# Optimization experiments

Measured on AMD Instinct MI355X. Metric: run time of the kernel, lower is better.

## Reference

```python
import jax, jax.numpy as jnp
import numpy as np
from jax import lax

B, CIN, L = 2048, 1024, 30
E, C = 8, 2            # num_experts, num_classes
FC_IN = 256 * 9        # 2304
FIN_IN = C + 512 * L + 256 * (L // 2 + 1)  # 19458


def _maxpool1d(x):
    # MaxPool1d(kernel=2, stride=2, padding=1); pad with -inf like torch
    return lax.reduce_window(x, -jnp.inf, lax.max,
                             (1, 1, 2), (1, 1, 2),
                             [(0, 0), (0, 0), (1, 1)])


def _conv1d(x, w):
    # x: [B,Cin,L], w: [Cout,Cin,3], padding=1
    return lax.conv_general_dilated(x, w, (1,), [(1, 1)],
                                    dimension_numbers=('NCH', 'OIH', 'NCH'))


def setup_inputs() -> dict:
    key = jax.random.key(0)
    ks = jax.random.split(key, 16)
    s = 0.02
    inp = {
        'x': jax.random.normal(ks[0], (B, CIN, L), jnp.float32),
        'expert_idx': jax.random.randint(ks[1], (B,), 0, E),
        'conv1_w': jax.random.normal(ks[2], (512, 1024, 3), jnp.float32) * s,
        'conv1_b': jnp.zeros((512,), jnp.float32),
        'conv2_w': jax.random.normal(ks[3], (256, 512, 3), jnp.float32) * s,
        'conv2_b': jnp.zeros((256,), jnp.float32),
        'fc_w': jax.random.normal(ks[4], (1024, FC_IN), jnp.float32) * s,
        'fc_b': jnp.zeros((1024,), jnp.float32),
        'e_w1': jax.random.normal(ks[5], (E, 512, 1024), jnp.float32) * s,
        'e_b1': jnp.zeros((E, 512), jnp.float32),
        'e_w2': jax.random.normal(ks[6], (E, C, 512), jnp.float32) * s,
        'e_b2': jnp.zeros((E, C), jnp.float32),
        'agg_w': jax.random.normal(ks[7], (C, E * C), jnp.float32) * s,
        'agg_b': jnp.zeros((C,), jnp.float32),
        'fin_w': jax.random.normal(ks[8], (C, FIN_IN), jnp.float32) * s,
        'fin_b': jnp.zeros((C,), jnp.float32),
    }
    return inp


def reference(x, expert_idx, conv1_w, conv1_b, conv2_w, conv2_b, fc_w, fc_b,
              e_w1, e_b1, e_w2, e_b2, agg_w, agg_b, fin_w, fin_b):
    b = x.shape[0]
    # shared feature extractor
    x1 = jax.nn.relu(_conv1d(x, conv1_w) + conv1_b[None, :, None])     # [B,512,30]
    p1 = _maxpool1d(x1)                                                 # [B,512,16]
    x2 = jax.nn.relu(_conv1d(p1, conv2_w) + conv2_b[None, :, None])    # [B,256,16]
    p2 = _maxpool1d(x2)                                                 # [B,256,9]
    sf = jax.nn.relu(p2.reshape(b, -1) @ fc_w.T + fc_b)                 # [B,1024]

    # expert dispatch: run all experts densely, then select per-sample
    h = jax.nn.relu(jnp.einsum('bd,ehd->beh', sf, e_w1) + e_b1)        # [B,E,512]
    all_out = jnp.einsum('beh,ech->bec', h, e_w2) + e_b2               # [B,E,C]
    sel = all_out[jnp.arange(b), expert_idx]                           # [B,C]
    oh = jax.nn.one_hot(expert_idx, E, dtype=sel.dtype)                # [B,E]
    expert_outputs = (oh[:, :, None] * sel[:, None, :]).reshape(b, E * C)

    agg = expert_outputs @ agg_w.T + agg_b                             # [B,C]
    combined = jnp.concatenate(
        [agg, x1.reshape(b, -1), x2.reshape(b, -1)], axis=1)           # [B,19458]
    return combined @ fin_w.T + fin_b                                  # [B,C]
```

## Files before the change

kernel.cpp:

```cpp
#include <hip/hip_runtime.h>
#include <hip/hip_bf16.h>

typedef short short8 __attribute__((ext_vector_type(8)));
typedef short short4v __attribute__((ext_vector_type(4)));
typedef float f32x4 __attribute__((ext_vector_type(4)));

__device__ __forceinline__ float bf2f(short s) {
  return __builtin_bit_cast(float, (unsigned)((unsigned short)s) << 16);
}
__device__ __forceinline__ short f2bf(float f) {
  return __builtin_bit_cast(short, __float2bfloat16(f));
}
__device__ __forceinline__ void g2lds16(const void* g, void* l) {
  __builtin_amdgcn_global_load_lds((const __attribute__((address_space(1))) void*)g,
                                   (__attribute__((address_space(3))) void*)l, 16, 0, 0);
}


__global__ __launch_bounds__(256) void prep_x(const float* __restrict__ x, short* __restrict__ xt) {
  __shared__ float tile[64 * 30];
  const int b = blockIdx.x, ci0 = blockIdx.y * 64, t = threadIdx.x;
  const float* src = x + ((long)b * 1024 + ci0) * 30;
  for (int i = t; i < 480; i += 256)
    ((float4*)tile)[i] = ((const float4*)src)[i];
  __syncthreads();
  short* dst = xt + (long)b * 32 * 1024 + ci0;
  for (int i = t; i < 512; i += 256) {
    int lp = i >> 4, cq = i & 15;
    short4v v = {0, 0, 0, 0};
    if (lp >= 1 && lp <= 30) {
#pragma unroll
      for (int u = 0; u < 4; ++u) v[u] = f2bf(tile[(cq * 4 + u) * 30 + lp - 1]);
    }
    *(short4v*)&dst[(long)lp * 1024 + cq * 4] = v;
  }
}

__global__ __launch_bounds__(256) void prep_weights(
    const float* __restrict__ conv1_w, const float* __restrict__ conv2_w,
    const float* __restrict__ fc_w, const float* __restrict__ e_w1,
    const float* __restrict__ fin_w,
    short* __restrict__ w1t, short* __restrict__ w2t, short* __restrict__ fcwt,
    short* __restrict__ ew1t, float* __restrict__ finw1, float* __restrict__ finw2) {
  const int T0 = 1572864;
  const int T1 = T0 + 393216;
  const int T2 = T1 + 2359296;
  const int T3 = T2 + 4194304;
  const int T4 = T3 + 30720;
  const int T5 = T4 + 8192;
  for (long idx = (long)blockIdx.x * 256 + threadIdx.x; idx < T5;
       idx += (long)gridDim.x * 256) {
    if (idx < T0) {
      int i = (int)idx; int co = i / 3072, j = i % 3072, k = j >> 10, ci = j & 1023;
      w1t[i] = f2bf(conv1_w[(co * 1024 + ci) * 3 + k]);
    } else if (idx < T1) {
      int i = (int)(idx - T0); int co = i / 1536, j = i % 1536, k = j >> 9, ci = j & 511;
      w2t[i] = f2bf(conv2_w[(co * 512 + ci) * 3 + k]);
    } else if (idx < T2) {
      int i = (int)(idx - T1); int n = i / 2304, j = i % 2304, jj = j >> 8, co = j & 255;
      fcwt[i] = f2bf(fc_w[n * 2304 + co * 9 + jj]);
    } else if (idx < T3) {
      int i = (int)(idx - T2);
      ew1t[i] = f2bf(e_w1[i]);
    } else if (idx < T4) {
      int i = (int)(idx - T3); int c = i / 15360, r = i % 15360, l = r >> 9, co = r & 511;
      finw1[i] = fin_w[c * 19458 + 2 + co * 30 + l];
    } else {
      int i = (int)(idx - T4); int c = i / 4096, r = i % 4096, l = r >> 8, co = r & 255;
      finw2[i] = fin_w[c * 19458 + 2 + 15360 + co * 16 + l];
    }
  }
}

__global__ __launch_bounds__(512, 2) void gemm256_bt_relu(
    const short* __restrict__ A, const short* __restrict__ Bm, short* __restrict__ C,
    const float* __restrict__ bias, int N, int K, int L, int S1, int S2, int nNB) {
  __shared__ __align__(16) short lA0[256 * 64], lA1[256 * 64];
  __shared__ __align__(16) short lB0[256 * 64], lB1[256 * 64];
  const int t = threadIdx.x, wave = t >> 6, lane = t & 63;
  const int wr = wave >> 2, wc = wave & 3;
  const int nwg = gridDim.x, qn = nwg >> 3, bid = blockIdx.x;
  const int swz = (bid & 7) * qn + (bid >> 3);
  const int m0 = (swz / nNB) * 256, n0 = (swz % nNB) * 256;
  const int srow = t >> 3;
  const int scol = (((t & 7) ^ (srow & 7)) * 8);

  long aoff[4], boff[4];
#pragma unroll
  for (int q = 0; q < 4; ++q) {
    int m = m0 + q * 64 + srow;
    aoff[q] = (long)(m / L) * S1 + (long)(m % L) * S2 + scol;
    boff[q] = (long)(n0 + q * 64 + srow) * K + scol;
  }
  const int ldst = wave * 512 + lane * 8;

  f32x4 acc[8][4];
#pragma unroll
  for (int i = 0; i < 8; ++i)
#pragma unroll
    for (int j = 0; j < 4; ++j) acc[i][j] = f32x4{0.f, 0.f, 0.f, 0.f};

  const int l7 = lane & 7, g4 = lane >> 4, r16 = lane & 15;
  const int nK = K >> 6;

#define STAGE256(k0, dA, dB) do {                                     \
    const long kk0_ = (long)(k0);                                     \
    _Pragma("unroll")                                                 \
    for (int q = 0; q < 4; ++q) {                                     \
      g2lds16(A + aoff[q] + kk0_, &dA[q * 4096 + ldst]);              \
      g2lds16(Bm + boff[q] + kk0_, &dB[q * 4096 + ldst]);             \
    } } while (0)

#define PHASES256(sA, sB) do {                                                        \
    short8 af[4][2], bfr[4][2];                                                       \
                                 \
    _Pragma("unroll") for (int kk = 0; kk < 2; ++kk) {                                \
      const int jb = ((kk * 4 + g4) ^ l7) * 8;                                        \
      _Pragma("unroll") for (int i = 0; i < 4; ++i)                                   \
        af[i][kk] = *(const short8*)&sA[(wr * 128 + i * 16 + r16) * 64 + jb];         \
      _Pragma("unroll") for (int j = 0; j < 2; ++j)                                   \
        bfr[j][kk] = *(const short8*)&sB[(wc * 64 + j * 16 + r16) * 64 + jb];         \
    }                                                                                 \
    __builtin_amdgcn_s_setprio(1);                                                    \
    _Pragma("unroll") for (int i = 0; i < 4; ++i)                                     \
    _Pragma("unroll") for (int j = 0; j < 2; ++j)                                     \
    _Pragma("unroll") for (int kk = 0; kk < 2; ++kk)                                  \
      acc[i][j] = __builtin_amdgcn_mfma_f32_16x16x32_bf16(af[i][kk], bfr[j][kk], acc[i][j], 0, 0, 0); \
    __builtin_amdgcn_s_setprio(0);                                                    \
                                         \
    _Pragma("unroll") for (int kk = 0; kk < 2; ++kk) {                                \
      const int jb = ((kk * 4 + g4) ^ l7) * 8;                                        \
      _Pragma("unroll") for (int j = 0; j < 2; ++j)                                   \
        bfr[2 + j][kk] = *(const short8*)&sB[(wc * 64 + (2 + j) * 16 + r16) * 64 + jb]; \
    }                                                                                 \
    __builtin_amdgcn_s_setprio(1);                                                    \
    _Pragma("unroll") for (int i = 0; i < 4; ++i)                                     \
    _Pragma("unroll") for (int j = 0; j < 2; ++j)                                     \
    _Pragma("unroll") for (int kk = 0; kk < 2; ++kk)                                  \
      acc[i][2 + j] = __builtin_amdgcn_mfma_f32_16x16x32_bf16(af[i][kk], bfr[2 + j][kk], acc[i][2 + j], 0, 0, 0); \
    __builtin_amdgcn_s_setprio(0);                                                    \
                                         \
    _Pragma("unroll") for (int kk = 0; kk < 2; ++kk) {                                \
      const int jb = ((kk * 4 + g4) ^ l7) * 8;                                        \
      _Pragma("unroll") for (int i = 0; i < 4; ++i)                                   \
        af[i][kk] = *(const short8*)&sA[(wr * 128 + (4 + i) * 16 + r16) * 64 + jb];   \
    }                                                                                 \
    __builtin_amdgcn_s_setprio(1);                                                    \
    _Pragma("unroll") for (int i = 0; i < 4; ++i)                                     \
    _Pragma("unroll") for (int j = 0; j < 2; ++j)                                     \
    _Pragma("unroll") for (int kk = 0; kk < 2; ++kk)                                  \
      acc[4 + i][2 + j] = __builtin_amdgcn_mfma_f32_16x16x32_bf16(af[i][kk], bfr[2 + j][kk], acc[4 + i][2 + j], 0, 0, 0); \
    __builtin_amdgcn_s_setprio(0);                                                    \
                                \
    __builtin_amdgcn_s_setprio(1);                                                    \
    _Pragma("unroll") for (int i = 0; i < 4; ++i)                                     \
    _Pragma("unroll") for (int j = 0; j < 2; ++j)                                     \
    _Pragma("unroll") for (int kk = 0; kk < 2; ++kk)                                  \
      acc[4 + i][j] = __builtin_amdgcn_mfma_f32_16x16x32_bf16(af[i][kk], bfr[j][kk], acc[4 + i][j], 0, 0, 0); \
    __builtin_amdgcn_s_setprio(0);                                                    \
  } while (0)

  STAGE256(0, lA0, lB0);
  for (int ktp = 0; ktp < (nK >> 1); ++ktp) {
    const int t1 = 2 * ktp + 1;
    __syncthreads();
    STAGE256((long)t1 << 6, lA1, lB1);
    PHASES256(lA0, lB0);
    __syncthreads();
    if (t1 + 1 < nK) STAGE256((long)(t1 + 1) << 6, lA0, lB0);
    PHASES256(lA1, lB1);
  }

#pragma unroll
  for (int j = 0; j < 4; ++j) {
    int col = n0 + wc * 64 + j * 16 + r16;
    float bv = bias[col];
#pragma unroll
    for (int i = 0; i < 8; ++i) {
      int rbase = m0 + wr * 128 + i * 16 + (g4 << 2);
#pragma unroll
      for (int r = 0; r < 4; ++r) {
        float o = fmaxf(acc[i][j][r] + bv, 0.f);
        C[(long)(rbase + r) * N + col] = f2bf(o);
      }
    }
  }
#undef STAGE256
#undef PHASES256
}

__global__ __launch_bounds__(256, 2) void gemm128_bt_relu(
    const short* __restrict__ A, const short* __restrict__ Bm, short* __restrict__ C,
    const float* __restrict__ bias, int N, int K, int L, int S1, int S2, int nNB) {
  __shared__ __align__(16) short lA0[128 * 64], lA1[128 * 64];
  __shared__ __align__(16) short lB0[128 * 64], lB1[128 * 64];
  const int t = threadIdx.x, wave = t >> 6, lane = t & 63;
  const int wr = wave >> 1, wc = wave & 1;
  const int nwg = gridDim.x, qn = nwg >> 3, bid = blockIdx.x;
  const int swz = (bid & 7) * qn + (bid >> 3);
  const int m0 = (swz / nNB) * 128, n0 = (swz % nNB) * 128;
  const int arow = t >> 3;
  const int acolg = (((t & 7) ^ (arow & 7)) * 8);

  long aoff[4], boff[4];
#pragma unroll
  for (int qq = 0; qq < 4; ++qq) {
    int m = m0 + qq * 32 + arow;
    aoff[qq] = (long)(m / L) * S1 + (long)(m % L) * S2 + acolg;
    boff[qq] = (long)(n0 + qq * 32 + arow) * K + acolg;
  }
  const int ldst = wave * 512 + lane * 8;

  f32x4 acc[4][4];
#pragma unroll
  for (int i = 0; i < 4; ++i)
#pragma unroll
    for (int j = 0; j < 4; ++j) acc[i][j] = f32x4{0.f, 0.f, 0.f, 0.f};

  const int l7 = lane & 7, g4 = lane >> 4, r16 = lane & 15;
  const int nK = K >> 6;

#define STAGE128(k0, dA, dB) do {                                     \
    const long kk0_ = (long)(k0);                                     \
    _Pragma("unroll")                                                 \
    for (int qq = 0; qq < 4; ++qq) {                                  \
      g2lds16(A + aoff[qq] + kk0_, &dA[qq * 2048 + ldst]);            \
      g2lds16(Bm + boff[qq] + kk0_, &dB[qq * 2048 + ldst]);           \
    } } while (0)

#define PHASES128(sA, sB) do {                                                        \
    _Pragma("unroll")                                                                 \
    for (int kk = 0; kk < 2; ++kk) {                                                  \
      const int jblk = ((kk * 4 + g4) ^ l7) * 8;                                      \
      short8 af[4], bfv[4];                                                           \
      _Pragma("unroll") for (int i = 0; i < 4; ++i)                                   \
        af[i] = *(const short8*)&sA[(wr * 64 + i * 16 + r16) * 64 + jblk];            \
      _Pragma("unroll") for (int j = 0; j < 4; ++j)                                   \
        bfv[j] = *(const short8*)&sB[(wc * 64 + j * 16 + r16) * 64 + jblk];           \
      __builtin_amdgcn_s_setprio(1);                                                  \
      _Pragma("unroll") for (int i = 0; i < 4; ++i)                                   \
      _Pragma("unroll") for (int j = 0; j < 4; ++j)                                   \
        acc[i][j] = __builtin_amdgcn_mfma_f32_16x16x32_bf16(af[i], bfv[j], acc[i][j], 0, 0, 0); \
      __builtin_amdgcn_s_setprio(0);                                                  \
    } } while (0)

  STAGE128(0, lA0, lB0);
  for (int ktp = 0; ktp < (nK >> 1); ++ktp) {
    const int t1 = 2 * ktp + 1;
    __syncthreads();
    STAGE128((long)t1 << 6, lA1, lB1);
    PHASES128(lA0, lB0);
    __syncthreads();
    if (t1 + 1 < nK) STAGE128((long)(t1 + 1) << 6, lA0, lB0);
    PHASES128(lA1, lB1);
  }

#pragma unroll
  for (int j = 0; j < 4; ++j) {
    int col = n0 + wc * 64 + j * 16 + r16;
    float bv = bias[col];
#pragma unroll
    for (int i = 0; i < 4; ++i) {
      int rbase = m0 + wr * 64 + i * 16 + (g4 << 2);
#pragma unroll
      for (int r = 0; r < 4; ++r) {
        float o = fmaxf(acc[i][j][r] + bv, 0.f);
        C[(long)(rbase + r) * N + col] = f2bf(o);
      }
    }
  }
#undef STAGE128
#undef PHASES128
}

__global__ __launch_bounds__(256) void pool1(const short* __restrict__ x1t, short* __restrict__ p1t) {
  const long total = (long)2048 * 18 * 128;
  for (long idx = (long)blockIdx.x * 256 + threadIdx.x; idx < total;
       idx += (long)gridDim.x * 256) {
    int c4 = (int)(idx & 127); long tmp = idx >> 7; int jp = (int)(tmp % 18); long b = tmp / 18;
    short4v v = {0, 0, 0, 0};
    if (jp >= 1 && jp <= 16) {
      int j = jp - 1;
      int l0 = 2 * j - 1, l1 = 2 * j;
      short4v a = (l0 >= 0) ? *(const short4v*)&x1t[(b * 30 + l0) * 512 + c4 * 4] : short4v{0, 0, 0, 0};
      short4v bb = (l1 < 30) ? *(const short4v*)&x1t[(b * 30 + l1) * 512 + c4 * 4] : short4v{0, 0, 0, 0};
#pragma unroll
      for (int u = 0; u < 4; ++u) v[u] = f2bf(fmaxf(bf2f(a[u]), bf2f(bb[u])));
    }
    *(short4v*)&p1t[idx * 4] = v;
  }
}

__global__ __launch_bounds__(256) void pool2(const short* __restrict__ x2t, short* __restrict__ p2t) {
  const long total = (long)2048 * 9 * 64;
  for (long idx = (long)blockIdx.x * 256 + threadIdx.x; idx < total;
       idx += (long)gridDim.x * 256) {
    int c4 = (int)(idx & 63); long tmp = idx >> 6; int j = (int)(tmp % 9); long b = tmp / 9;
    int l0 = 2 * j - 1, l1 = 2 * j;
    short4v a = (l0 >= 0) ? *(const short4v*)&x2t[(b * 16 + l0) * 256 + c4 * 4] : short4v{0, 0, 0, 0};
    short4v bb = (l1 < 16) ? *(const short4v*)&x2t[(b * 16 + l1) * 256 + c4 * 4] : short4v{0, 0, 0, 0};
    short4v v;
#pragma unroll
    for (int u = 0; u < 4; ++u) v[u] = f2bf(fmaxf(bf2f(a[u]), bf2f(bb[u])));
    *(short4v*)&p2t[idx * 4] = v;
  }
}

__global__ __launch_bounds__(256) void final_k(
    const short* __restrict__ h, const short* __restrict__ x1t, const short* __restrict__ x2t,
    const int* __restrict__ eidx, const float* __restrict__ e_w2, const float* __restrict__ e_b2,
    const float* __restrict__ agg_w, const float* __restrict__ agg_b,
    const float* __restrict__ fin_w, const float* __restrict__ fin_b,
    const float* __restrict__ finw1, const float* __restrict__ finw2,
    float* __restrict__ out) {
  const int b = blockIdx.x, t = threadIdx.x, lane = t & 63, wave = t >> 6;
  const int e = eidx[b];
  float s0 = 0.f, s1 = 0.f, f0 = 0.f, f1 = 0.f;
  {
    const short* hp = h + (long)b * 4096 + e * 512;
    const float* w20 = e_w2 + (e * 2 + 0) * 512;
    const float* w21 = e_w2 + (e * 2 + 1) * 512;
    for (int i = t; i < 512; i += 256) {
      float hv = bf2f(hp[i]);
      s0 += hv * w20[i];
      s1 += hv * w21[i];
    }
  }
  {
    const short* xp = x1t + (long)b * 15360;
#pragma unroll
    for (int it = 0; it < 15; ++it) {
      int i = (it * 256 + t) * 4;
      short4v xv = *(const short4v*)&xp[i];
      float4 w0 = *(const float4*)&finw1[i];
      float4 w1 = *(const float4*)&finw1[15360 + i];
      float a0 = bf2f(xv[0]), a1 = bf2f(xv[1]), a2 = bf2f(xv[2]), a3 = bf2f(xv[3]);
      f0 += a0 * w0.x + a1 * w0.y + a2 * w0.z + a3 * w0.w;
      f1 += a0 * w1.x + a1 * w1.y + a2 * w1.z + a3 * w1.w;
    }
    const short* x2p = x2t + (long)b * 4096;
#pragma unroll
    for (int it = 0; it < 4; ++it) {
      int i = (it * 256 + t) * 4;
      short4v xv = *(const short4v*)&x2p[i];
      float4 w0 = *(const float4*)&finw2[i];
      float4 w1 = *(const float4*)&finw2[4096 + i];
      float a0 = bf2f(xv[0]), a1 = bf2f(xv[1]), a2 = bf2f(xv[2]), a3 = bf2f(xv[3]);
      f0 += a0 * w0.x + a1 * w0.y + a2 * w0.z + a3 * w0.w;
      f1 += a0 * w1.x + a1 * w1.y + a2 * w1.z + a3 * w1.w;
    }
  }
#pragma unroll
  for (int off = 32; off > 0; off >>= 1) {
    s0 += __shfl_down(s0, off);
    s1 += __shfl_down(s1, off);
    f0 += __shfl_down(f0, off);
    f1 += __shfl_down(f1, off);
  }
  __shared__ float red[4][4];
  if (lane == 0) { red[wave][0] = s0; red[wave][1] = s1; red[wave][2] = f0; red[wave][3] = f1; }
  __syncthreads();
  if (t == 0) {
    float S0 = 0, S1 = 0, F0 = 0, F1 = 0;
    for (int w = 0; w < 4; ++w) { S0 += red[w][0]; S1 += red[w][1]; F0 += red[w][2]; F1 += red[w][3]; }
    float sel0 = S0 + e_b2[e * 2 + 0];
    float sel1 = S1 + e_b2[e * 2 + 1];
    float agg0 = sel0 * agg_w[e * 2] + sel1 * agg_w[e * 2 + 1] + agg_b[0];
    float agg1 = sel0 * agg_w[16 + e * 2] + sel1 * agg_w[16 + e * 2 + 1] + agg_b[1];
    out[b * 2 + 0] = F0 + agg0 * fin_w[0] + agg1 * fin_w[1] + fin_b[0];
    out[b * 2 + 1] = F1 + agg0 * fin_w[19458 + 0] + agg1 * fin_w[19458 + 1] + fin_b[1];
  }
}

extern "C" void kernel_launch(void* const* d_in, const int* in_sizes, int n_in,
                              void* d_out, int out_size, void* d_ws, size_t ws_size,
                              hipStream_t stream) {
  const float* x       = (const float*)d_in[0];
  const int*   eidx    = (const int*)d_in[1];
  const float* conv1_w = (const float*)d_in[2];
  const float* conv1_b = (const float*)d_in[3];
  const float* conv2_w = (const float*)d_in[4];
  const float* conv2_b = (const float*)d_in[5];
  const float* fc_w    = (const float*)d_in[6];
  const float* fc_b    = (const float*)d_in[7];
  const float* e_w1    = (const float*)d_in[8];
  const float* e_b1    = (const float*)d_in[9];
  const float* e_w2    = (const float*)d_in[10];
  const float* e_b2    = (const float*)d_in[11];
  const float* agg_w   = (const float*)d_in[12];
  const float* agg_b   = (const float*)d_in[13];
  const float* fin_w   = (const float*)d_in[14];
  const float* fin_b   = (const float*)d_in[15];
  float* out = (float*)d_out;

  char* ws = (char*)d_ws;
  short* xt    = (short*)(ws + 0L);
  short* x1t   = (short*)(ws + 134217728L);
  short* p1t   = (short*)(ws + 197132288L);
  short* x2t   = (short*)(ws + 234881024L);
  short* p2t   = (short*)(ws + 251658240L);
  short* sf    = (short*)(ws + 261095424L);
  short* h     = (short*)(ws + 265289728L);
  short* w1t   = (short*)(ws + 282066944L);
  short* w2t   = (short*)(ws + 285212672L);
  short* fcwt  = (short*)(ws + 285999104L);
  short* ew1t  = (short*)(ws + 290717696L);
  float* finw1 = (float*)(ws + 299106304L);
  float* finw2 = (float*)(ws + 299229184L);

  prep_weights<<<4096, 256, 0, stream>>>(conv1_w, conv2_w, fc_w, e_w1, fin_w,
                                         w1t, w2t, fcwt, ew1t, finw1, finw2);
  prep_x<<<dim3(2048, 16), 256, 0, stream>>>(x, xt);
  gemm256_bt_relu<<<480, 512, 0, stream>>>(xt, w1t, x1t, conv1_b, 512, 3072, 30, 32768, 1024, 2);
  pool1<<<2048, 256, 0, stream>>>(x1t, p1t);
  gemm128_bt_relu<<<512, 256, 0, stream>>>(p1t, w2t, x2t, conv2_b, 256, 1536, 16, 9216, 512, 2);
  pool2<<<1024, 256, 0, stream>>>(x2t, p2t);
  gemm128_bt_relu<<<128, 256, 0, stream>>>(p2t, fcwt, sf, fc_b, 1024, 2304, 1, 2304, 0, 8);
  gemm128_bt_relu<<<512, 256, 0, stream>>>(sf, ew1t, h, e_b1, 4096, 1024, 1, 1024, 0, 32);
  final_k<<<2048, 256, 0, stream>>>(h, x1t, x2t, eidx, e_w2, e_b2, agg_w, agg_b,
                                    fin_w, fin_b, finw1, finw2, out);
}
```

Measured before the change: 398.0 us.

## Load conv1 GEMM B operand directly to registers; fuse final-layer dots into pooling kernels

The conv1 GEMM no longer stages the weight (B) tile through LDS. Each wave now loads its B fragments straight from global memory into registers, which halves LDS use and removes the B LDS reads. Separately, the final linear layer's dot products over x1 and x2 move into the pooling kernels, which already read those activations, so x1 and x2 are not reread by the final kernel. The final kernel shrinks to a single wave doing only the expert head. The risks are that the uncoalesced global B loads now sit on the MFMA critical path, and that fin1p/fin2p reuse workspace offset 0, which aliases the xt buffer that is already consumed by then.

Result: slower. 527.4 us (+32.5%).

```diff
diff --git a/kernel.cpp b/kernel.cpp
--- a/kernel.cpp
+++ b/kernel.cpp
@@ -76,7 +76,6 @@
     const short* __restrict__ A, const short* __restrict__ Bm, short* __restrict__ C,
     const float* __restrict__ bias, int N, int K, int L, int S1, int S2, int nNB) {
   __shared__ __align__(16) short lA0[256 * 64], lA1[256 * 64];
-  __shared__ __align__(16) short lB0[256 * 64], lB1[256 * 64];
   const int t = threadIdx.x, wave = t >> 6, lane = t & 63;
   const int wr = wave >> 2, wc = wave & 3;
   const int nwg = gridDim.x, qn = nwg >> 3, bid = blockIdx.x;
@@ -85,41 +84,51 @@
   const int srow = t >> 3;
   const int scol = (((t & 7) ^ (srow & 7)) * 8);
 
-  long aoff[4], boff[4];
+  long aoff[4];
 #pragma unroll
   for (int q = 0; q < 4; ++q) {
     int m = m0 + q * 64 + srow;
     aoff[q] = (long)(m / L) * S1 + (long)(m % L) * S2 + scol;
-    boff[q] = (long)(n0 + q * 64 + srow) * K + scol;
   }
   const int ldst = wave * 512 + lane * 8;
 
+  const int l7 = lane & 7, g4 = lane >> 4, r16 = lane & 15;
+  long brow[4];
+#pragma unroll
+  for (int j = 0; j < 4; ++j)
+    brow[j] = (long)(n0 + wc * 64 + j * 16 + r16) * K + g4 * 8;
+
   f32x4 acc[8][4];
 #pragma unroll
   for (int i = 0; i < 8; ++i)
 #pragma unroll
     for (int j = 0; j < 4; ++j) acc[i][j] = f32x4{0.f, 0.f, 0.f, 0.f};
 
-  const int l7 = lane & 7, g4 = lane >> 4, r16 = lane & 15;
   const int nK = K >> 6;
-
-#define STAGE256(k0, dA, dB) do {                                     \
+  short8 bfr[4][2];
+
+#define STAGEA(k0, dA) do {                                           \
     const long kk0_ = (long)(k0);                                     \
     _Pragma("unroll")                                                 \
-    for (int q = 0; q < 4; ++q) {                                     \
+    for (int q = 0; q < 4; ++q)                                       \
       g2lds16(A + aoff[q] + kk0_, &dA[q * 4096 + ldst]);              \
-      g2lds16(Bm + boff[q] + kk0_, &dB[q * 4096 + ldst]);             \
-    } } while (0)
-
-#define PHASES256(sA, sB) do {                                                        \
-    short8 af[4][2], bfr[4][2];                                                       \
-                                 \
+    } while (0)
+
+#define LOADB(k0) do {                                                \
+    const long kb_ = (long)(k0);                                      \
+    _Pragma("unroll") for (int j = 0; j < 4; ++j)                     \
+    _Pragma("unroll") for (int kk = 0; kk < 2; ++kk)                  \
+      bfr[j][kk] = *(const short8*)&Bm[brow[j] + kb_ + kk * 32];      \
+    __builtin_amdgcn_sched_barrier(0);                                \
+    } while (0)
+
+#define PHASESB(sA) do {                                                              \
+    short8 af[4][2];                                                                  \
+                                            \
     _Pragma("unroll") for (int kk = 0; kk < 2; ++kk) {                                \
       const int jb = ((kk * 4 + g4) ^ l7) * 8;                                        \
       _Pragma("unroll") for (int i = 0; i < 4; ++i)                                   \
         af[i][kk] = *(const short8*)&sA[(wr * 128 + i * 16 + r16) * 64 + jb];         \
-      _Pragma("unroll") for (int j = 0; j < 2; ++j)                                   \
-        bfr[j][kk] = *(const short8*)&sB[(wc * 64 + j * 16 + r16) * 64 + jb];         \
     }                                                                                 \
     __builtin_amdgcn_s_setprio(1);                                                    \
     _Pragma("unroll") for (int i = 0; i < 4; ++i)                                     \
@@ -127,19 +136,14 @@
     _Pragma("unroll") for (int kk = 0; kk < 2; ++kk)                                  \
       acc[i][j] = __builtin_amdgcn_mfma_f32_16x16x32_bf16(af[i][kk], bfr[j][kk], acc[i][j], 0, 0, 0); \
     __builtin_amdgcn_s_setprio(0);                                                    \
-                                         \
-    _Pragma("unroll") for (int kk = 0; kk < 2; ++kk) {                                \
-      const int jb = ((kk * 4 + g4) ^ l7) * 8;                                        \
-      _Pragma("unroll") for (int j = 0; j < 2; ++j)                                   \
-        bfr[2 + j][kk] = *(const short8*)&sB[(wc * 64 + (2 + j) * 16 + r16) * 64 + jb]; \
-    }                                                                                 \
+                                                       \
     __builtin_amdgcn_s_setprio(1);                                                    \
     _Pragma("unroll") for (int i = 0; i < 4; ++i)                                     \
     _Pragma("unroll") for (int j = 0; j < 2; ++j)                                     \
     _Pragma("unroll") for (int kk = 0; kk < 2; ++kk)                                  \
       acc[i][2 + j] = __builtin_amdgcn_mfma_f32_16x16x32_bf16(af[i][kk], bfr[2 + j][kk], acc[i][2 + j], 0, 0, 0); \
     __builtin_amdgcn_s_setprio(0);                                                    \
-                                         \
+                                            \
     _Pragma("unroll") for (int kk = 0; kk < 2; ++kk) {                                \
       const int jb = ((kk * 4 + g4) ^ l7) * 8;                                        \
       _Pragma("unroll") for (int i = 0; i < 4; ++i)                                   \
@@ -151,7 +155,7 @@
     _Pragma("unroll") for (int kk = 0; kk < 2; ++kk)                                  \
       acc[4 + i][2 + j] = __builtin_amdgcn_mfma_f32_16x16x32_bf16(af[i][kk], bfr[2 + j][kk], acc[4 + i][2 + j], 0, 0, 0); \
     __builtin_amdgcn_s_setprio(0);                                                    \
-                                \
+                                                       \
     __builtin_amdgcn_s_setprio(1);                                                    \
     _Pragma("unroll") for (int i = 0; i < 4; ++i)                                     \
     _Pragma("unroll") for (int j = 0; j < 2; ++j)                                     \
@@ -160,15 +164,17 @@
     __builtin_amdgcn_s_setprio(0);                                                    \
   } while (0)
 
-  STAGE256(0, lA0, lB0);
+  STAGEA(0, lA0);
   for (int ktp = 0; ktp < (nK >> 1); ++ktp) {
     const int t1 = 2 * ktp + 1;
     __syncthreads();
-    STAGE256((long)t1 << 6, lA1, lB1);
-    PHASES256(lA0, lB0);
+    LOADB((long)(2 * ktp) << 6);
+    STAGEA((long)t1 << 6, lA1);
+    PHASESB(lA0);
     __syncthreads();
-    if (t1 + 1 < nK) STAGE256((long)(t1 + 1) << 6, lA0, lB0);
-    PHASES256(lA1, lB1);
+    LOADB((long)t1 << 6);
+    if (t1 + 1 < nK) STAGEA((long)(t1 + 1) << 6, lA0);
+    PHASESB(lA1);
   }
 
 #pragma unroll
@@ -185,8 +191,9 @@
       }
     }
   }
-#undef STAGE256
-#undef PHASES256
+#undef STAGEA
+#undef LOADB
+#undef PHASESB
 }
 
 __global__ __launch_bounds__(256, 2) void gemm128_bt_relu(
@@ -273,100 +280,124 @@
 #undef PHASES128
 }
 
-__global__ __launch_bounds__(256) void pool1(const short* __restrict__ x1t, short* __restrict__ p1t) {
-  const long total = (long)2048 * 18 * 128;
-  for (long idx = (long)blockIdx.x * 256 + threadIdx.x; idx < total;
-       idx += (long)gridDim.x * 256) {
-    int c4 = (int)(idx & 127); long tmp = idx >> 7; int jp = (int)(tmp % 18); long b = tmp / 18;
+__global__ __launch_bounds__(256) void pool1_fused(
+    const short* __restrict__ x1t, short* __restrict__ p1t,
+    const float* __restrict__ finw1, float* __restrict__ fin1p) {
+  const int b = blockIdx.x, t = threadIdx.x, lane = t & 63, wave = t >> 6;
+  const short* xb = x1t + (long)b * 15360;
+  short* pb = p1t + (long)b * 9216;
+  for (int i = t; i < 2304; i += 256) {
+    int c4 = i & 127, jp = i >> 7;
     short4v v = {0, 0, 0, 0};
     if (jp >= 1 && jp <= 16) {
-      int j = jp - 1;
-      int l0 = 2 * j - 1, l1 = 2 * j;
-      short4v a = (l0 >= 0) ? *(const short4v*)&x1t[(b * 30 + l0) * 512 + c4 * 4] : short4v{0, 0, 0, 0};
-      short4v bb = (l1 < 30) ? *(const short4v*)&x1t[(b * 30 + l1) * 512 + c4 * 4] : short4v{0, 0, 0, 0};
+      int j = jp - 1, l0 = 2 * j - 1, l1 = 2 * j;
+      short4v a = (l0 >= 0) ? *(const short4v*)&xb[l0 * 512 + c4 * 4] : short4v{0, 0, 0, 0};
+      short4v bb = (l1 < 30) ? *(const short4v*)&xb[l1 * 512 + c4 * 4] : short4v{0, 0, 0, 0};
 #pragma unroll
       for (int u = 0; u < 4; ++u) v[u] = f2bf(fmaxf(bf2f(a[u]), bf2f(bb[u])));
     }
-    *(short4v*)&p1t[idx * 4] = v;
-  }
-}
-
-__global__ __launch_bounds__(256) void pool2(const short* __restrict__ x2t, short* __restrict__ p2t) {
-  const long total = (long)2048 * 9 * 64;
-  for (long idx = (long)blockIdx.x * 256 + threadIdx.x; idx < total;
-       idx += (long)gridDim.x * 256) {
-    int c4 = (int)(idx & 63); long tmp = idx >> 6; int j = (int)(tmp % 9); long b = tmp / 9;
+    *(short4v*)&pb[i * 4] = v;
+  }
+  float f0 = 0.f, f1 = 0.f;
+#pragma unroll
+  for (int it = 0; it < 15; ++it) {
+    int i = (it * 256 + t) * 4;
+    short4v xv = *(const short4v*)&xb[i];
+    float4 w0 = *(const float4*)&finw1[i];
+    float4 w1 = *(const float4*)&finw1[15360 + i];
+    float a0 = bf2f(xv[0]), a1 = bf2f(xv[1]), a2 = bf2f(xv[2]), a3 = bf2f(xv[3]);
+    f0 += a0 * w0.x + a1 * w0.y + a2 * w0.z + a3 * w0.w;
+    f1 += a0 * w1.x + a1 * w1.y + a2 * w1.z + a3 * w1.w;
+  }
+#pragma unroll
+  for (int off = 32; off > 0; off >>= 1) {
+    f0 += __shfl_down(f0, off);
+    f1 += __shfl_down(f1, off);
+  }
+  __shared__ float red[4][2];
+  if (lane == 0) { red[wave][0] = f0; red[wave][1] = f1; }
+  __syncthreads();
+  if (t == 0) {
+    float F0 = red[0][0] + red[1][0] + red[2][0] + red[3][0];
+    float F1 = red[0][1] + red[1][1] + red[2][1] + red[3][1];
+    fin1p[b * 2 + 0] = F0;
+    fin1p[b * 2 + 1] = F1;
+  }
+}
+
+__global__ __launch_bounds__(256) void pool2_fused(
+    const short* __restrict__ x2t, short* __restrict__ p2t,
+    const float* __restrict__ finw2, float* __restrict__ fin2p) {
+  const int b = blockIdx.x, t = threadIdx.x, lane = t & 63, wave = t >> 6;
+  const short* xb = x2t + (long)b * 4096;
+  short* pb = p2t + (long)b * 2304;
+  for (int i = t; i < 576; i += 256) {
+    int c4 = i & 63, j = i >> 6;
     int l0 = 2 * j - 1, l1 = 2 * j;
-    short4v a = (l0 >= 0) ? *(const short4v*)&x2t[(b * 16 + l0) * 256 + c4 * 4] : short4v{0, 0, 0, 0};
-    short4v bb = (l1 < 16) ? *(const short4v*)&x2t[(b * 16 + l1) * 256 + c4 * 4] : short4v{0, 0, 0, 0};
+    short4v a = (l0 >= 0) ? *(const short4v*)&xb[l0 * 256 + c4 * 4] : short4v{0, 0, 0, 0};
+    short4v bb = (l1 < 16) ? *(const short4v*)&xb[l1 * 256 + c4 * 4] : short4v{0, 0, 0, 0};
     short4v v;
 #pragma unroll
     for (int u = 0; u < 4; ++u) v[u] = f2bf(fmaxf(bf2f(a[u]), bf2f(bb[u])));
-    *(short4v*)&p2t[idx * 4] = v;
-  }
-}
-
-__global__ __launch_bounds__(256) void final_k(
-    const short* __restrict__ h, const short* __restrict__ x1t, const short* __restrict__ x2t,
-    const int* __restrict__ eidx, const float* __restrict__ e_w2, const float* __restrict__ e_b2,
+    *(short4v*)&pb[i * 4] = v;
+  }
+  float f0 = 0.f, f1 = 0.f;
+#pragma unroll
+  for (int it = 0; it < 4; ++it) {
+    int i = (it * 256 + t) * 4;
+    short4v xv = *(const short4v*)&xb[i];
+    float4 w0 = *(const float4*)&finw2[i];
+    float4 w1 = *(const float4*)&finw2[4096 + i];
+    float a0 = bf2f(xv[0]), a1 = bf2f(xv[1]), a2 = bf2f(xv[2]), a3 = bf2f(xv[3]);
+    f0 += a0 * w0.x + a1 * w0.y + a2 * w0.z + a3 * w0.w;
+    f1 += a0 * w1.x + a1 * w1.y + a2 * w1.z + a3 * w1.w;
+  }
+#pragma unroll
+  for (int off = 32; off > 0; off >>= 1) {
+    f0 += __shfl_down(f0, off);
+    f1 += __shfl_down(f1, off);
+  }
+  __shared__ float red[4][2];
+  if (lane == 0) { red[wave][0] = f0; red[wave][1] = f1; }
+  __syncthreads();
+  if (t == 0) {
+    fin2p[b * 2 + 0] = red[0][0] + red[1][0] + red[2][0] + red[3][0];
+    fin2p[b * 2 + 1] = red[0][1] + red[1][1] + red[2][1] + red[3][1];
+  }
+}
+
+__global__ __launch_bounds__(64) void final_k(
+    const short* __restrict__ h, const int* __restrict__ eidx,
+    const float* __restrict__ e_w2, const float* __restrict__ e_b2,
     const float* __restrict__ agg_w, const float* __restrict__ agg_b,
     const float* __restrict__ fin_w, const float* __restrict__ fin_b,
-    const float* __restrict__ finw1, const float* __restrict__ finw2,
+    const float* __restrict__ fin1p, const float* __restrict__ fin2p,
     float* __restrict__ out) {
-  const int b = blockIdx.x, t = threadIdx.x, lane = t & 63, wave = t >> 6;
+  const int b = blockIdx.x, lane = threadIdx.x;
   const int e = eidx[b];
-  float s0 = 0.f, s1 = 0.f, f0 = 0.f, f1 = 0.f;
-  {
-    const short* hp = h + (long)b * 4096 + e * 512;
-    const float* w20 = e_w2 + (e * 2 + 0) * 512;
-    const float* w21 = e_w2 + (e * 2 + 1) * 512;
-    for (int i = t; i < 512; i += 256) {
-      float hv = bf2f(hp[i]);
-      s0 += hv * w20[i];
-      s1 += hv * w21[i];
-    }
-  }
-  {
-    const short* xp = x1t + (long)b * 15360;
-#pragma unroll
-    for (int it = 0; it < 15; ++it) {
-      int i = (it * 256 + t) * 4;
-      short4v xv = *(const short4v*)&xp[i];
-      float4 w0 = *(const float4*)&finw1[i];
-      float4 w1 = *(const float4*)&finw1[15360 + i];
-      float a0 = bf2f(xv[0]), a1 = bf2f(xv[1]), a2 = bf2f(xv[2]), a3 = bf2f(xv[3]);
-      f0 += a0 * w0.x + a1 * w0.y + a2 * w0.z + a3 * w0.w;
-      f1 += a0 * w1.x + a1 * w1.y + a2 * w1.z + a3 * w1.w;
-    }
-    const short* x2p = x2t + (long)b * 4096;
-#pragma unroll
-    for (int it = 0; it < 4; ++it) {
-      int i = (it * 256 + t) * 4;
-      short4v xv = *(const short4v*)&x2p[i];
-      float4 w0 = *(const float4*)&finw2[i];
-      float4 w1 = *(const float4*)&finw2[4096 + i];
-      float a0 = bf2f(xv[0]), a1 = bf2f(xv[1]), a2 = bf2f(xv[2]), a3 = bf2f(xv[3]);
-      f0 += a0 * w0.x + a1 * w0.y + a2 * w0.z + a3 * w0.w;
-      f1 += a0 * w1.x + a1 * w1.y + a2 * w1.z + a3 * w1.w;
-    }
+  const short* hp = h + (long)b * 4096 + e * 512;
+  const float* w20 = e_w2 + (e * 2 + 0) * 512;
+  const float* w21 = e_w2 + (e * 2 + 1) * 512;
+  float s0 = 0.f, s1 = 0.f;
+#pragma unroll
+  for (int it = 0; it < 8; ++it) {
+    int i = it * 64 + lane;
+    float hv = bf2f(hp[i]);
+    s0 += hv * w20[i];
+    s1 += hv * w21[i];
   }
 #pragma unroll
   for (int off = 32; off > 0; off >>= 1) {
     s0 += __shfl_down(s0, off);
     s1 += __shfl_down(s1, off);
-    f0 += __shfl_down(f0, off);
-    f1 += __shfl_down(f1, off);
-  }
-  __shared__ float red[4][4];
-  if (lane == 0) { red[wave][0] = s0; red[wave][1] = s1; red[wave][2] = f0; red[wave][3] = f1; }
-  __syncthreads();
-  if (t == 0) {
-    float S0 = 0, S1 = 0, F0 = 0, F1 = 0;
-    for (int w = 0; w < 4; ++w) { S0 += red[w][0]; S1 += red[w][1]; F0 += red[w][2]; F1 += red[w][3]; }
-    float sel0 = S0 + e_b2[e * 2 + 0];
-    float sel1 = S1 + e_b2[e * 2 + 1];
+  }
+  if (lane == 0) {
+    float sel0 = s0 + e_b2[e * 2 + 0];
+    float sel1 = s1 + e_b2[e * 2 + 1];
     float agg0 = sel0 * agg_w[e * 2] + sel1 * agg_w[e * 2 + 1] + agg_b[0];
     float agg1 = sel0 * agg_w[16 + e * 2] + sel1 * agg_w[16 + e * 2 + 1] + agg_b[1];
+    float F0 = fin1p[b * 2 + 0] + fin2p[b * 2 + 0];
+    float F1 = fin1p[b * 2 + 1] + fin2p[b * 2 + 1];
     out[b * 2 + 0] = F0 + agg0 * fin_w[0] + agg1 * fin_w[1] + fin_b[0];
     out[b * 2 + 1] = F1 + agg0 * fin_w[19458 + 0] + agg1 * fin_w[19458 + 1] + fin_b[1];
   }
@@ -407,16 +438,18 @@
   short* ew1t  = (short*)(ws + 290717696L);
   float* finw1 = (float*)(ws + 299106304L);
   float* finw2 = (float*)(ws + 299229184L);
+  float* fin1p = (float*)(ws + 0L);
+  float* fin2p = (float*)(ws + 16384L);
 
   prep_weights<<<4096, 256, 0, stream>>>(conv1_w, conv2_w, fc_w, e_w1, fin_w,
                                          w1t, w2t, fcwt, ew1t, finw1, finw2);
   prep_x<<<dim3(2048, 16), 256, 0, stream>>>(x, xt);
   gemm256_bt_relu<<<480, 512, 0, stream>>>(xt, w1t, x1t, conv1_b, 512, 3072, 30, 32768, 1024, 2);
-  pool1<<<2048, 256, 0, stream>>>(x1t, p1t);
+  pool1_fused<<<2048, 256, 0, stream>>>(x1t, p1t, finw1, fin1p);
   gemm128_bt_relu<<<512, 256, 0, stream>>>(p1t, w2t, x2t, conv2_b, 256, 1536, 16, 9216, 512, 2);
-  pool2<<<1024, 256, 0, stream>>>(x2t, p2t);
+  pool2_fused<<<2048, 256, 0, stream>>>(x2t, p2t, finw2, fin2p);
   gemm128_bt_relu<<<128, 256, 0, stream>>>(p2t, fcwt, sf, fc_b, 1024, 2304, 1, 2304, 0, 8);
   gemm128_bt_relu<<<512, 256, 0, stream>>>(sf, ew1t, h, e_b1, 4096, 1024, 1, 1024, 0, 32);
-  final_k<<<2048, 256, 0, stream>>>(h, x1t, x2t, eidx, e_w2, e_b2, agg_w, agg_b,
-                                    fin_w, fin_b, finw1, finw2, out);
-}
+  final_k<<<2048, 64, 0, stream>>>(h, eidx, e_w2, e_b2, agg_w, agg_b,
+                                   fin_w, fin_b, fin1p, fin2p, out);
+}
```
